# Optimization experiments

Hardware: AMD Instinct MI355X
Metric: run time of the kernel (lower is better)

The kernel has to match this reference:

```python
import jax, jax.numpy as jnp
import numpy as np

L, B, S, D, H, F = 3, 2, 2048, 256, 8, 1024
DK = D // H
EPS = 1e-7


def _positional_encoding(max_len: int, dim: int) -> jnp.ndarray:
    # pos in [1, max_len], i in [1, dim]; w = pos / 10000**((2*i//2)/dim) == pos / 10000**(i/dim)
    pos = np.arange(1, max_len + 1, dtype=np.float64)[:, None]
    i = np.arange(1, dim + 1)
    w = pos / np.power(10000.0, i.astype(np.float64) / dim)[None, :]
    pe = np.where((i % 2 == 0)[None, :], np.sin(w), np.cos(w))
    return jnp.asarray(pe, jnp.float32)


def _ln(x, g, b):
    mu = jnp.mean(x, axis=-1, keepdims=True)
    var = jnp.mean((x - mu) ** 2, axis=-1, keepdims=True)
    return (x - mu) / jnp.sqrt(var + EPS) * g + b


def setup_inputs() -> dict:
    key = jax.random.key(0)
    ks = jax.random.split(key, 16)
    s = 0.05
    inp = {
        "x": jax.random.normal(ks[0], (B, S, D), jnp.float32),
        "mask": jax.random.randint(ks[1], (B, S, S), 0, 2).astype(bool),
        "pe": _positional_encoding(S, D),
        "Wq": jax.random.normal(ks[2], (L, H, D, DK), jnp.float32) * s,
        "Wk": jax.random.normal(ks[3], (L, H, D, DK), jnp.float32) * s,
        "Wv": jax.random.normal(ks[4], (L, H, D, DK), jnp.float32) * s,
        "Wo": jax.random.normal(ks[5], (L, D, D), jnp.float32) * s,
        "bo": jnp.zeros((L, D), jnp.float32),
        "ln1_g": jnp.ones((L, D), jnp.float32),
        "ln1_b": jnp.zeros((L, D), jnp.float32),
        "W1": jax.random.normal(ks[6], (L, D, F), jnp.float32) * s,
        "b1": jnp.zeros((L, F), jnp.float32),
        "W2": jax.random.normal(ks[7], (L, F, D), jnp.float32) * s,
        "b2": jnp.zeros((L, D), jnp.float32),
        "ln2_g": jnp.ones((L, D), jnp.float32),
        "ln2_b": jnp.zeros((L, D), jnp.float32),
    }
    return inp


def _encoder_layer(x, mask, Wq, Wk, Wv, Wo, bo, ln1_g, ln1_b, W1, b1, W2, b2, ln2_g, ln2_b):
    # all heads batched: [B,S,D] x [H,D,dk] -> [B,H,S,dk]
    q = jnp.einsum('bsd,hdk->bhsk', x, Wq)
    k = jnp.einsum('bsd,hdk->bhsk', x, Wk)
    v = jnp.einsum('bsd,hdk->bhsk', x, Wv)
    scores = jnp.einsum('bhsk,bhtk->bhst', q, k) / jnp.sqrt(jnp.float32(DK))
    neg = -jnp.finfo(jnp.float32).max
    scores = jnp.where(mask[:, None, :, :], neg, scores)
    attn = jax.nn.softmax(scores, axis=-1)
    # concat heads along feature dim (head-major order as torch.cat dim=2)
    o = jnp.einsum('bhst,bhtv->bshv', attn, v).reshape(x.shape[0], x.shape[1], D)
    o = o @ Wo + bo
    x = _ln(o + x, ln1_g, ln1_b)  # post-norm (prenorm=False), dropout_rate=0
    h = jax.nn.relu(x @ W1 + b1) @ W2 + b2
    x = _ln(h + x, ln2_g, ln2_b)
    return x


def reference(x, mask, pe, Wq, Wk, Wv, Wo, bo, ln1_g, ln1_b, W1, b1, W2, b2, ln2_g, ln2_b):
    x = x + pe[None, : x.shape[1], :]
    for l in range(L):
        x = _encoder_layer(x, mask, Wq[l], Wk[l], Wv[l], Wo[l], bo[l], ln1_g[l], ln1_b[l],
                           W1[l], b1[l], W2[l], b2[l], ln2_g[l], ln2_b[l])
    return x
```

## Files before the change

### kernel.cpp

```cpp
#include <hip/hip_runtime.h>
#include <hip/hip_bf16.h>
#include <cfloat>

#define Lc 3
#define Bc 2
#define Sc 2048
#define Dc 256
#define Hc 8
#define DKc 32
#define Fc 1024

typedef __hip_bfloat16 bf16;
typedef short s8v __attribute__((ext_vector_type(8)));
typedef float f4v __attribute__((ext_vector_type(4)));

#define QSCALE 0.25504526036067815f

#if __has_builtin(__builtin_amdgcn_exp2f)
#define EXP2(x) __builtin_amdgcn_exp2f(x)
#else
#define EXP2(x) exp2f(x)
#endif

__device__ __forceinline__ float load_f(const void* p, size_t i, int isbf)
{
    return isbf ? __bfloat162float(((const bf16*)p)[i]) : ((const float*)p)[i];
}

typedef const __attribute__((address_space(1))) char gchar_t;
typedef __attribute__((address_space(3))) char lchar_t;
__device__ __forceinline__ void glds16(const void* g, void* l)
{
    __builtin_amdgcn_global_load_lds((gchar_t*)(size_t)g, (lchar_t*)(size_t)l,
                                     16, 0, 0);
}

#define NBLK_REPACK 2304
#define NBLK_CONV   6942
#define NBLK_PACK   1024
#define NBLK_PE     4096

__global__ __launch_bounds__(256) void prologue_fused(
    const void* __restrict__ x, const void* __restrict__ mask,
    const void* __restrict__ pe,
    const void* Wq, const void* Wk, const void* Wv,
    const void* Wo, const void* W1, const void* W2,
    const void* bo, const void* b1, const void* b2,
    const void* g1, const void* be1, const void* g2, const void* be2,
    bf16* __restrict__ wqkv, bf16* __restrict__ dstb, float* __restrict__ pc,
    unsigned* __restrict__ pmask, float* __restrict__ xf,
    bf16* __restrict__ xb, int* __restrict__ flags)
{
    __shared__ int sf[2];
    int tid = threadIdx.x;
    if (tid < 64) {
        const unsigned short* u16 = (const unsigned short*)x;
        int cnt = 0;
        for (int i = tid; i < 256; i += 64) {
            unsigned e = (u16[2 * i] >> 7) & 0xFF;
            cnt += (e >= 90 && e <= 140) ? 1 : 0;
        }
        #pragma unroll
        for (int d = 1; d < 64; d <<= 1) cnt += __shfl_xor(cnt, d);
        const unsigned* mu = (const unsigned*)mask;
        int c2 = ((mu[tid] & 0xFFFFFF00u) == 0) ? 1 : 0;
        #pragma unroll
        for (int d = 1; d < 64; d <<= 1) c2 += __shfl_xor(c2, d);
        if (tid == 0) {
            sf[0] = (cnt >= 128) ? 1 : 0;
            sf[1] = (c2 >= 48) ? 1 : 0;
            if (blockIdx.x == 0) { flags[0] = sf[0]; flags[1] = sf[1]; }
        }
    }
    __syncthreads();
    int isbf = sf[0], mf = sf[1];
    int blk = blockIdx.x;

    if (blk < NBLK_REPACK) {
        int idx = blk * 256 + tid;
        int l   = idx / (3 * Dc * Dc);
        int rem = idx % (3 * Dc * Dc);
        int col = rem / Dc;
        int d   = rem % Dc;
        int mat = col / Dc;
        int hk  = col % Dc;
        int h = hk / DKc, kk = hk % DKc;
        const void* W = (mat == 0) ? Wq : (mat == 1) ? Wk : Wv;
        float v = load_f(W, (size_t)l * (Hc * Dc * DKc) + h * (Dc * DKc) + d * DKc + kk, isbf);
        wqkv[idx] = __float2bfloat16(v);
    } else if (blk < NBLK_REPACK + NBLK_CONV) {
        const int NB0 = Lc * Dc * Dc;
        const int NB1 = NB0 + Lc * Dc * Fc;
        const int NB2 = NB1 + Lc * Fc * Dc;
        int idx = (blk - NBLK_REPACK) * 256 + tid;
        if (idx < NB2) {
            const void* src; int off;
            if (idx < NB0) {
                int l = idx / (Dc * Dc); int rem = idx % (Dc * Dc);
                int n = rem / Dc, k = rem % Dc;
                src = Wo; off = l * Dc * Dc + k * Dc + n;
            } else if (idx < NB1) {
                int j = idx - NB0;
                int l = j / (Fc * Dc); int rem = j % (Fc * Dc);
                int n = rem / Dc, k = rem % Dc;
                src = W1; off = l * Dc * Fc + k * Fc + n;
            } else {
                int j = idx - NB1;
                int l = j / (Dc * Fc); int rem = j % (Dc * Fc);
                int n = rem / Fc, k = rem % Fc;
                src = W2; off = l * Fc * Dc + k * Dc + n;
            }
            dstb[idx] = __float2bfloat16(load_f(src, off, isbf));
        } else {
            int off = idx - NB2;
            if (off < 7680) {
                const void* src; int lo;
                if (off < 768)       { src = bo;  lo = off; }
                else if (off < 3840) { src = b1;  lo = off - 768; }
                else if (off < 4608) { src = b2;  lo = off - 3840; }
                else if (off < 5376) { src = g1;  lo = off - 4608; }
                else if (off < 6144) { src = be1; lo = off - 5376; }
                else if (off < 6912) { src = g2;  lo = off - 6144; }
                else                 { src = be2; lo = off - 6912; }
                pc[off] = load_f(src, lo, isbf);
            }
        }
    } else if (blk < NBLK_REPACK + NBLK_CONV + NBLK_PACK) {
        int idx = (blk - NBLK_REPACK - NBLK_CONV) * 256 + tid;
        unsigned wb = 0;
        if (mf) {
            const int* mp = (const int*)mask + (size_t)idx * 32;
            #pragma unroll
            for (int u = 0; u < 8; ++u) {
                uint4 q = *(const uint4*)(mp + u * 4);
                wb |= (q.x ? 1u : 0u) << (u * 4);
                wb |= (q.y ? 1u : 0u) << (u * 4 + 1);
                wb |= (q.z ? 1u : 0u) << (u * 4 + 2);
                wb |= (q.w ? 1u : 0u) << (u * 4 + 3);
            }
        } else {
            const unsigned char* mp = (const unsigned char*)mask + (size_t)idx * 32;
            uint4 a = *(const uint4*)mp;
            uint4 bq = *(const uint4*)(mp + 16);
            const unsigned char* ab = (const unsigned char*)&a;
            const unsigned char* bb = (const unsigned char*)&bq;
            #pragma unroll
            for (int j = 0; j < 16; ++j) {
                wb |= (ab[j] ? 1u : 0u) << j;
                wb |= (bb[j] ? 1u : 0u) << (16 + j);
            }
        }
        pmask[idx] = wb;
    } else {
        int idx = (blk - NBLK_REPACK - NBLK_CONV - NBLK_PACK) * 256 + tid;
        int rem = idx % (Sc * Dc);
        float v = load_f(x, idx, isbf) + load_f(pe, rem, isbf);
        xf[idx] = v;
        xb[idx] = __float2bfloat16(v);
    }
}

__global__ __launch_bounds__(256) void gemm_mfma(
    const bf16* __restrict__ A, const bf16* __restrict__ BT,
    const float* __restrict__ bias, void* __restrict__ C,
    bf16* __restrict__ vt,
    int M, int N, int K, int relu, int obf, float ascale, int scale_ncols,
    int ldc)
{
    __shared__ __align__(16) short As[2][4096];
    __shared__ __align__(16) short Bs[2][4096];
    int tid = threadIdx.x;
    int w = tid >> 6, lane = tid & 63;
    int quad = lane >> 4, l15 = lane & 15;
    int wm0 = (w & 1) * 32, wn0 = (w >> 1) * 32;
    int row0 = blockIdx.y * 64, col0 = blockIdx.x * 64;

    int s0 = w * 128 + lane;
    int s1 = s0 + 64;
    int r0 = s0 >> 3, c0 = ((s0 & 7) ^ (r0 & 7)) * 8;
    int r1 = s1 >> 3, c1 = ((s1 & 7) ^ (r1 & 7)) * 8;
    const bf16* Ag0 = A + (size_t)(row0 + r0) * K + c0;
    const bf16* Ag1 = A + (size_t)(row0 + r1) * K + c1;
    const bf16* Bg0 = BT + (size_t)(col0 + r0) * K + c0;
    const bf16* Bg1 = BT + (size_t)(col0 + r1) * K + c1;

    f4v acc00 = {0.f,0.f,0.f,0.f}, acc01 = acc00, acc10 = acc00, acc11 = acc00;

    int m0 = wm0 + l15, m1 = wm0 + 16 + l15;
    int n0 = wn0 + l15, n1 = wn0 + 16 + l15;
    int sw7 = l15 & 7;

#define GSTAGE(bi, kk) do { \
        glds16(Ag0 + (kk), As[bi] + w * 1024); \
        glds16(Ag1 + (kk), As[bi] + w * 1024 + 512); \
        glds16(Bg0 + (kk), Bs[bi] + w * 1024); \
        glds16(Bg1 + (kk), Bs[bi] + w * 1024 + 512); \
    } while (0)

    GSTAGE(0, 0);
    for (int k0 = 0; k0 < K; k0 += 64) {
        int cur = (k0 >> 6) & 1;
        __syncthreads();
        if (k0 + 64 < K) GSTAGE(cur ^ 1, k0 + 64);
        const short* Ab = As[cur];
        const short* Bb = Bs[cur];
        #pragma unroll
        for (int kc = 0; kc < 2; ++kc) {
            int sw = ((kc * 4 + quad) ^ sw7) * 8;
            s8v a0 = *(const s8v*)(Ab + m0 * 64 + sw);
            s8v a1 = *(const s8v*)(Ab + m1 * 64 + sw);
            s8v b0 = *(const s8v*)(Bb + n0 * 64 + sw);
            s8v b1 = *(const s8v*)(Bb + n1 * 64 + sw);
            acc00 = __builtin_amdgcn_mfma_f32_16x16x32_bf16(a0, b0, acc00, 0, 0, 0);
            acc01 = __builtin_amdgcn_mfma_f32_16x16x32_bf16(a0, b1, acc01, 0, 0, 0);
            acc10 = __builtin_amdgcn_mfma_f32_16x16x32_bf16(a1, b0, acc10, 0, 0, 0);
            acc11 = __builtin_amdgcn_mfma_f32_16x16x32_bf16(a1, b1, acc11, 0, 0, 0);
        }
    }
#undef GSTAGE

    f4v accs[2][2] = {{acc00, acc01}, {acc10, acc11}};

    if (vt && col0 >= 2 * Dc) {
        __syncthreads();
        #pragma unroll
        for (int mt = 0; mt < 2; ++mt) {
            #pragma unroll
            for (int nt = 0; nt < 2; ++nt) {
                int lc = wn0 + nt * 16 + l15;
                #pragma unroll
                for (int reg = 0; reg < 4; ++reg) {
                    int lr = wm0 + mt * 16 + quad * 4 + reg;
                    int p = ((lr & 15) << 2) | (lr >> 4);
                    bf16 bv = __float2bfloat16(accs[mt][nt][reg]);
                    As[0][lc * 64 + (p ^ ((lc & 7) << 3))] = *(short*)&bv;
                }
            }
        }
        __syncthreads();
        int bI = row0 >> 11;
        int srow = row0 & (Sc - 1);
        #pragma unroll
        for (int j = 0; j < 2; ++j) {
            int e = j * 256 + tid;
            int c = e >> 3, p0 = (e & 7) * 8;
            s8v vv = *(const s8v*)(As[0] + c * 64 + (p0 ^ ((c & 7) << 3)));
            int gcv = col0 - 2 * Dc + c;
            size_t vb = ((size_t)(bI * Hc + (gcv >> 5)) * DKc + (gcv & 31)) * Sc
                        + srow + p0;
            *(s8v*)(vt + vb) = vv;
        }
        return;
    }

    float bv0 = bias ? bias[col0 + wn0 + l15] : 0.f;
    float bv1 = bias ? bias[col0 + wn0 + 16 + l15] : 0.f;
    #pragma unroll
    for (int mt = 0; mt < 2; ++mt) {
        #pragma unroll
        for (int nt = 0; nt < 2; ++nt) {
            int gr = row0 + wm0 + mt * 16 + quad * 4;
            int gc = col0 + wn0 + nt * 16 + l15;
            float badd = nt ? bv1 : bv0;
            float sc = (gc < scale_ncols) ? ascale : 1.f;
            #pragma unroll
            for (int reg = 0; reg < 4; ++reg) {
                float v = accs[mt][nt][reg] * sc + badd;
                if (relu) v = fmaxf(v, 0.f);
                if (obf) ((bf16*)C)[(size_t)(gr + reg) * ldc + gc] = __float2bfloat16(v);
                else     ((float*)C)[(size_t)(gr + reg) * ldc + gc] = v;
            }
        }
    }
}

__global__ __launch_bounds__(256) void gemm_mfma32(
    const bf16* __restrict__ A, const bf16* __restrict__ BT,
    const float* __restrict__ bias, void* __restrict__ C,
    int M, int N, int K, int relu, int obf)
{
    __shared__ __align__(16) short As[2][2048];
    __shared__ __align__(16) short Bs[2][4096];
    int tid = threadIdx.x;
    int w = tid >> 6, lane = tid & 63;
    int quad = lane >> 4, l15 = lane & 15;
    int wm0 = (w & 1) * 16, wn0 = (w >> 1) * 32;
    int row0 = blockIdx.y * 32, col0 = blockIdx.x * 64;

    int sa = w * 64 + lane;
    int ra = sa >> 3, ca = ((sa & 7) ^ (ra & 7)) * 8;
    int s0 = w * 128 + lane, s1 = s0 + 64;
    int r0 = s0 >> 3, c0 = ((s0 & 7) ^ (r0 & 7)) * 8;
    int r1 = s1 >> 3, c1 = ((s1 & 7) ^ (r1 & 7)) * 8;
    const bf16* Ag  = A + (size_t)(row0 + ra) * K + ca;
    const bf16* Bg0 = BT + (size_t)(col0 + r0) * K + c0;
    const bf16* Bg1 = BT + (size_t)(col0 + r1) * K + c1;

    f4v acc0 = {0.f,0.f,0.f,0.f}, acc1 = acc0;

    int m0 = wm0 + l15;
    int n0 = wn0 + l15, n1 = wn0 + 16 + l15;
    int sw7 = l15 & 7;

#define GSTAGE32(bi, kk) do { \
        glds16(Ag + (kk), As[bi] + w * 512); \
        glds16(Bg0 + (kk), Bs[bi] + w * 1024); \
        glds16(Bg1 + (kk), Bs[bi] + w * 1024 + 512); \
    } while (0)

    GSTAGE32(0, 0);
    for (int k0 = 0; k0 < K; k0 += 64) {
        int cur = (k0 >> 6) & 1;
        __syncthreads();
        if (k0 + 64 < K) GSTAGE32(cur ^ 1, k0 + 64);
        const short* Ab = As[cur];
        const short* Bb = Bs[cur];
        #pragma unroll
        for (int kc = 0; kc < 2; ++kc) {
            int sw = ((kc * 4 + quad) ^ sw7) * 8;
            s8v a0 = *(const s8v*)(Ab + m0 * 64 + sw);
            s8v b0 = *(const s8v*)(Bb + n0 * 64 + sw);
            s8v b1 = *(const s8v*)(Bb + n1 * 64 + sw);
            acc0 = __builtin_amdgcn_mfma_f32_16x16x32_bf16(a0, b0, acc0, 0, 0, 0);
            acc1 = __builtin_amdgcn_mfma_f32_16x16x32_bf16(a0, b1, acc1, 0, 0, 0);
        }
    }
#undef GSTAGE32

    float bv0 = bias ? bias[col0 + wn0 + l15] : 0.f;
    float bv1 = bias ? bias[col0 + wn0 + 16 + l15] : 0.f;
    f4v accs[2] = {acc0, acc1};
    #pragma unroll
    for (int nt = 0; nt < 2; ++nt) {
        int gr = row0 + wm0 + quad * 4;
        int gc = col0 + wn0 + nt * 16 + l15;
        float badd = nt ? bv1 : bv0;
        #pragma unroll
        for (int reg = 0; reg < 4; ++reg) {
            float v = accs[nt][reg] + badd;
            if (relu) v = fmaxf(v, 0.f);
            if (obf) ((bf16*)C)[(size_t)(gr + reg) * N + gc] = __float2bfloat16(v);
            else     ((float*)C)[(size_t)(gr + reg) * N + gc] = v;
        }
    }
}

__global__ __launch_bounds__(256) void flash_mfma(
    const bf16* __restrict__ qkv, const bf16* __restrict__ vt,
    const unsigned* __restrict__ pmask,
    bf16* __restrict__ op0, bf16* __restrict__ op1,
    bf16* __restrict__ op2, bf16* __restrict__ op3,
    float* __restrict__ spart)
{
    __shared__ __align__(16) short Ks[2][2048];
    __shared__ __align__(16) short Vs[2][2048];
    __shared__ __align__(16) short Pw[4][16 * 72];

    int tid = threadIdx.x;
    int w = tid >> 6;
    int lane = tid & 63;
    int quad = lane >> 4, l15 = lane & 15;
    int q0 = blockIdx.x * 64;
    int h = blockIdx.y;
    int z = blockIdx.z;
    int b = z >> 2, rng = z & 3;
    bf16* op = (rng == 0) ? op0 : (rng == 1) ? op1 : (rng == 2) ? op2 : op3;

    s8v qfrag = *(const s8v*)(qkv + (size_t)(b * Sc + q0 + w * 16 + l15) * 512 + h * 32 + quad * 8);

    int sr = tid >> 3, ss = tid & 7;
    int c8 = ss ^ (sr & 7);
    const bf16* kg = qkv + (size_t)(b * Sc + rng * (Sc / 4) + 2 * sr + (c8 >> 2)) * 512
                     + 256 + h * 32 + (c8 & 3) * 8;
    const bf16* vg = vt + ((size_t)(b * Hc + h) * DKc + sr) * Sc + rng * (Sc / 4) + c8 * 8;

    int koff = (l15 >> 1) * 64 + ((((l15 & 1) << 2) + quad) ^ ((l15 >> 1) & 7)) * 8;
    int pfoff = l15 * 72 + quad * 8;
    int vkey = l15 & 7;
    int voff = l15 * 64;

    f4v o0 = {0.f,0.f,0.f,0.f}, o1 = o0;
    float ssum[4] = {0.f, 0.f, 0.f, 0.f};

    short* pwv = Pw[w];
    const unsigned* mp = pmask + (size_t)b * Sc * (Sc / 32)
                         + (size_t)(q0 + w * 16 + quad * 4) * (Sc / 32) + rng * 16;

#define FSTAGE(bi, it2) do { \
        glds16(kg + (size_t)(it2) * (64 * 512), Ks[bi] + w * 512); \
        glds16(vg + (it2) * 64, Vs[bi] + w * 512); \
    } while (0)

    FSTAGE(0, 0);
    for (int it = 0; it < 8; ++it) {
        int cur = it & 1;
        __syncthreads();
        if (it < 7) FSTAGE(cur ^ 1, it + 1);

        uint2 mw[4];
        #pragma unroll
        for (int reg = 0; reg < 4; ++reg)
            mw[reg] = *(const uint2*)(mp + reg * (Sc / 32) + it * 2);

        const short* kb = Ks[cur];
        f4v sfr[4];
        __builtin_amdgcn_s_setprio(1);
        #pragma unroll
        for (int nt = 0; nt < 4; ++nt) {
            s8v kf = *(const s8v*)(kb + koff + nt * 512);
            f4v zz = {0.f,0.f,0.f,0.f};
            sfr[nt] = __builtin_amdgcn_mfma_f32_16x16x32_bf16(qfrag, kf, zz, 0, 0, 0);
        }
        __builtin_amdgcn_s_setprio(0);
        #pragma unroll
        for (int reg = 0; reg < 4; ++reg) {
            unsigned ta = mw[reg].x >> l15;
            unsigned tb = mw[reg].y >> l15;
            float p0 = EXP2(sfr[0][reg]); if (ta & 1u)         p0 = 0.f;
            float p1 = EXP2(sfr[1][reg]); if ((ta >> 16) & 1u) p1 = 0.f;
            float p2 = EXP2(sfr[2][reg]); if (tb & 1u)         p2 = 0.f;
            float p3 = EXP2(sfr[3][reg]); if ((tb >> 16) & 1u) p3 = 0.f;
            ssum[reg] += (p0 + p1) + (p2 + p3);
            __hip_bfloat162 plo = __float22bfloat162_rn(make_float2(p0, p1));
            __hip_bfloat162 phi = __float22bfloat162_rn(make_float2(p2, p3));
            uint2 pk = {*(unsigned*)&plo, *(unsigned*)&phi};
            *(uint2*)(pwv + (quad * 4 + reg) * 72 + l15 * 4) = pk;
        }
        const short* vb = Vs[cur];
        __builtin_amdgcn_s_setprio(1);
        #pragma unroll
        for (int kc = 0; kc < 2; ++kc) {
            s8v pf = *(const s8v*)(pwv + pfoff + kc * 32);
            int vo = voff + (((kc * 4 + quad) ^ vkey) * 8);
            s8v vf0 = *(const s8v*)(vb + vo);
            s8v vf1 = *(const s8v*)(vb + vo + 1024);
            o0 = __builtin_amdgcn_mfma_f32_16x16x32_bf16(pf, vf0, o0, 0, 0, 0);
            o1 = __builtin_amdgcn_mfma_f32_16x16x32_bf16(pf, vf1, o1, 0, 0, 0);
        }
        __builtin_amdgcn_s_setprio(0);
    }
#undef FSTAGE

    #pragma unroll
    for (int reg = 0; reg < 4; ++reg) {
        #pragma unroll
        for (int d = 1; d < 16; d <<= 1) ssum[reg] += __shfl_xor(ssum[reg], d);
    }

    #pragma unroll
    for (int reg = 0; reg < 4; ++reg) {
        int row = q0 + w * 16 + quad * 4 + reg;
        size_t ob = (size_t)(b * Sc + row) * Dc + h * DKc;
        op[ob + l15]      = __float2bfloat16(o0[reg]);
        op[ob + 16 + l15] = __float2bfloat16(o1[reg]);
        if (l15 == 0)
            spart[((size_t)(rng * Bc + b) * Hc + h) * Sc + row] = ssum[reg];
    }
}

__global__ __launch_bounds__(256) void attn_merge(
    const bf16* __restrict__ op0, const bf16* __restrict__ op1,
    const bf16* __restrict__ op2, const bf16* __restrict__ op3,
    const float* __restrict__ spart, bf16* __restrict__ attn_out)
{
    int t8 = blockIdx.x * 256 + threadIdx.x;
    size_t idx = (size_t)t8 * 8;
    int d = (int)(idx & 255);
    int h = d >> 5;
    int row = (int)((idx >> 8) & (Sc - 1));
    int b = (int)(idx >> 19);
    float s = 0.f;
    #pragma unroll
    for (int r = 0; r < 4; ++r)
        s += spart[((size_t)(r * Bc + b) * Hc + h) * Sc + row];
    float inv = 1.f / fmaxf(s, 1e-30f);

    uint4 a0 = *(const uint4*)(op0 + idx);
    uint4 a1 = *(const uint4*)(op1 + idx);
    uint4 a2 = *(const uint4*)(op2 + idx);
    uint4 a3 = *(const uint4*)(op3 + idx);
    const unsigned short* u0 = (const unsigned short*)&a0;
    const unsigned short* u1 = (const unsigned short*)&a1;
    const unsigned short* u2 = (const unsigned short*)&a2;
    const unsigned short* u3 = (const unsigned short*)&a3;
    unsigned short outv[8];
    #pragma unroll
    for (int j = 0; j < 8; ++j) {
        float o = (__uint_as_float((unsigned)u0[j] << 16) + __uint_as_float((unsigned)u1[j] << 16))
                + (__uint_as_float((unsigned)u2[j] << 16) + __uint_as_float((unsigned)u3[j] << 16));
        bf16 ov = __float2bfloat16(o * inv);
        outv[j] = *(unsigned short*)&ov;
    }
    *(uint4*)(attn_out + idx) = *(uint4*)outv;
}

__global__ __launch_bounds__(256) void add_ln(
    const float* __restrict__ a, float* __restrict__ xf, bf16* __restrict__ xb,
    const float* __restrict__ g, const float* __restrict__ b,
    void* __restrict__ dout, const int* __restrict__ flags)
{
    __shared__ float ws4[2][4];
    int row = blockIdx.x, d = threadIdx.x;
    size_t idx = (size_t)row * Dc + d;
    float v = a[idx] + xf[idx];
    float s = v;
    #pragma unroll
    for (int dd = 1; dd < 64; dd <<= 1) s += __shfl_xor(s, dd);
    if ((d & 63) == 0) ws4[0][d >> 6] = s;
    __syncthreads();
    float mu = (ws4[0][0] + ws4[0][1] + ws4[0][2] + ws4[0][3]) * (1.f / Dc);
    float c = v - mu;
    float q = c * c;
    #pragma unroll
    for (int dd = 1; dd < 64; dd <<= 1) q += __shfl_xor(q, dd);
    if ((d & 63) == 0) ws4[1][d >> 6] = q;
    __syncthreads();
    float var = (ws4[1][0] + ws4[1][1] + ws4[1][2] + ws4[1][3]) * (1.f / Dc);
    float r2 = c * rsqrtf(var + 1e-7f) * g[d] + b[d];
    xf[idx] = r2;
    xb[idx] = __float2bfloat16(r2);
    if (dout) {
        if (flags[0]) ((bf16*)dout)[idx] = __float2bfloat16(r2);
        else          ((float*)dout)[idx] = r2;
    }
}

extern "C" void kernel_launch(void* const* d_in, const int* in_sizes, int n_in,
                              void* d_out, int out_size, void* d_ws, size_t ws_size,
                              hipStream_t stream)
{
    const void* x    = d_in[0];
    const void* mask = d_in[1];
    const void* pe   = d_in[2];
    const void* Wq   = d_in[3];
    const void* Wk   = d_in[4];
    const void* Wv   = d_in[5];
    const void* Wo   = d_in[6];
    const void* bo   = d_in[7];
    const void* ln1g = d_in[8];
    const void* ln1b = d_in[9];
    const void* W1   = d_in[10];
    const void* b1   = d_in[11];
    const void* W2   = d_in[12];
    const void* b2   = d_in[13];
    const void* ln2g = d_in[14];
    const void* ln2b = d_in[15];

    const int M = Bc * Sc;
    char* ws = (char*)d_ws;
    const size_t MB = 1024 * 1024;
    int*      flags    = (int*)ws;
    float*    xf32     = (float*)(ws + 256);
    float*    obuf     = (float*)(ws + 256 + 4 * MB);
    char*     bigc     = ws + 256 + 8 * MB;
    bf16*     xbf      = (bf16*)(ws + 256 + 16 * MB);
    bf16*     attn_out = (bf16*)(ws + 256 + 18 * MB);
    bf16*     wqkv     = (bf16*)(ws + 256 + 20 * MB);
    bf16*     woc      = wqkv + (size_t)Lc * Dc * 3 * Dc;
    bf16*     w1c      = woc + (size_t)Lc * Dc * Dc;
    bf16*     w2c      = w1c + (size_t)Lc * Dc * Fc;
    float*    pc       = (float*)(w2c + (size_t)Lc * Fc * Dc);
    unsigned* pmask    = (unsigned*)(ws + 256 + 25 * MB);
    float*    spart    = (float*)(ws + 256 + 26 * MB);

    bf16* qkv  = (bf16*)bigc;
    bf16* vtb  = (bf16*)(bigc + 4 * MB);
    bf16* hbuf = (bf16*)bigc;
    bf16* op0  = (bf16*)obuf;
    bf16* op1  = op0 + (size_t)M * Dc;
    bf16* op2  = attn_out;
    bf16* op3  = (bf16*)(bigc + 6 * MB);

    float* pc_bo   = pc;
    float* pc_b1   = pc + 768;
    float* pc_b2   = pc + 3840;
    float* pc_ln1g = pc + 4608;
    float* pc_ln1b = pc + 5376;
    float* pc_ln2g = pc + 6144;
    float* pc_ln2b = pc + 6912;

    prologue_fused<<<NBLK_REPACK + NBLK_CONV + NBLK_PACK + NBLK_PE, 256, 0, stream>>>(
        x, mask, pe, Wq, Wk, Wv, Wo, W1, W2, bo, b1, b2,
        ln1g, ln1b, ln2g, ln2b, wqkv, woc, pc, pmask, xf32, xbf, flags);

    for (int l = 0; l < Lc; ++l) {
        gemm_mfma<<<dim3(3 * Dc / 64, M / 64), 256, 0, stream>>>(
            xbf, wqkv + (size_t)l * Dc * 3 * Dc, nullptr, qkv, vtb,
            M, 3 * Dc, Dc, 0, 1, QSCALE, Dc, 512);
        flash_mfma<<<dim3(Sc / 64, Hc, Bc * 4), 256, 0, stream>>>(
            qkv, vtb, pmask, op0, op1, op2, op3, spart);
        attn_merge<<<(Bc * Sc * Dc / 8) / 256, 256, 0, stream>>>(
            op0, op1, op2, op3, spart, attn_out);
        gemm_mfma32<<<dim3(Dc / 64, M / 32), 256, 0, stream>>>(
            attn_out, woc + (size_t)l * Dc * Dc, pc_bo + l * Dc, obuf, M, Dc, Dc, 0, 0);
        add_ln<<<M, 256, 0, stream>>>(obuf, xf32, xbf,
            pc_ln1g + l * Dc, pc_ln1b + l * Dc, nullptr, flags);
        gemm_mfma<<<dim3(Fc / 64, M / 64), 256, 0, stream>>>(
            xbf, w1c + (size_t)l * Dc * Fc, pc_b1 + l * Fc, hbuf, nullptr,
            M, Fc, Dc, 1, 1, 1.f, 0, Fc);
        gemm_mfma32<<<dim3(Dc / 64, M / 32), 256, 0, stream>>>(
            hbuf, w2c + (size_t)l * Fc * Dc, pc_b2 + l * Dc, obuf, M, Dc, Fc, 0, 0);
        add_ln<<<M, 256, 0, stream>>>(obuf, xf32, xbf,
            pc_ln2g + l * Dc, pc_ln2b + l * Dc,
            (l == Lc - 1) ? d_out : nullptr, flags);
    }
}
```

Baseline: 343.5 us.

## Triple-buffer K/V tiles in flash attention with explicit vmcnt waits and mask prefetch

Moves the flash attention K/V staging from a double buffer to a triple buffer, issuing loads two tiles ahead. It replaces __syncthreads with explicit s_waitcnt vmcnt counts plus a raw s_barrier, fully unrolls the loop, and prefetches the next tile's mask words into registers. The goal is to hide global-to-LDS latency and mask load latency behind MFMA work. In exchange it uses more LDS, which can lower occupancy. The hand-counted vmcnt values must match the real number of outstanding loads or the kernel will read stale data.

```diff
diff --git a/kernel.cpp b/kernel.cpp
--- a/kernel.cpp
+++ b/kernel.cpp
@@ -352,8 +352,8 @@
     bf16* __restrict__ op2, bf16* __restrict__ op3,
     float* __restrict__ spart)
 {
-    __shared__ __align__(16) short Ks[2][2048];
-    __shared__ __align__(16) short Vs[2][2048];
+    __shared__ __align__(16) short Ks[3][2048];
+    __shared__ __align__(16) short Vs[3][2048];
     __shared__ __align__(16) short Pw[4][16 * 72];
 
     int tid = threadIdx.x;
@@ -391,18 +391,29 @@
         glds16(vg + (it2) * 64, Vs[bi] + w * 512); \
     } while (0)
 
+    uint2 mwc[4], mwn[4];
+    #pragma unroll
+    for (int reg = 0; reg < 4; ++reg)
+        mwc[reg] = *(const uint2*)(mp + reg * (Sc / 32));
     FSTAGE(0, 0);
+    FSTAGE(1, 1);
+
+    #pragma unroll
     for (int it = 0; it < 8; ++it) {
-        int cur = it & 1;
-        __syncthreads();
-        if (it < 7) FSTAGE(cur ^ 1, it + 1);
-
-        uint2 mw[4];
-        #pragma unroll
-        for (int reg = 0; reg < 4; ++reg)
-            mw[reg] = *(const uint2*)(mp + reg * (Sc / 32) + it * 2);
-
-        const short* kb = Ks[cur];
+        if (it < 7) {
+            #pragma unroll
+            for (int reg = 0; reg < 4; ++reg)
+                mwn[reg] = *(const uint2*)(mp + reg * (Sc / 32) + (it + 1) * 2);
+            asm volatile("s_waitcnt vmcnt(6)" ::: "memory");
+        } else {
+            asm volatile("s_waitcnt vmcnt(0)" ::: "memory");
+        }
+        __builtin_amdgcn_sched_barrier(0);
+        __builtin_amdgcn_s_barrier();
+        __builtin_amdgcn_sched_barrier(0);
+        if (it + 2 < 8) FSTAGE((it + 2) % 3, it + 2);
+
+        const short* kb = Ks[it % 3];
         f4v sfr[4];
         __builtin_amdgcn_s_setprio(1);
         #pragma unroll
@@ -414,8 +425,8 @@
         __builtin_amdgcn_s_setprio(0);
         #pragma unroll
         for (int reg = 0; reg < 4; ++reg) {
-            unsigned ta = mw[reg].x >> l15;
-            unsigned tb = mw[reg].y >> l15;
+            unsigned ta = mwc[reg].x >> l15;
+            unsigned tb = mwc[reg].y >> l15;
             float p0 = EXP2(sfr[0][reg]); if (ta & 1u)         p0 = 0.f;
             float p1 = EXP2(sfr[1][reg]); if ((ta >> 16) & 1u) p1 = 0.f;
             float p2 = EXP2(sfr[2][reg]); if (tb & 1u)         p2 = 0.f;
@@ -426,7 +437,7 @@
             uint2 pk = {*(unsigned*)&plo, *(unsigned*)&phi};
             *(uint2*)(pwv + (quad * 4 + reg) * 72 + l15 * 4) = pk;
         }
-        const short* vb = Vs[cur];
+        const short* vb = Vs[it % 3];
         __builtin_amdgcn_s_setprio(1);
         #pragma unroll
         for (int kc = 0; kc < 2; ++kc) {
@@ -438,6 +449,8 @@
             o1 = __builtin_amdgcn_mfma_f32_16x16x32_bf16(pf, vf1, o1, 0, 0, 0);
         }
         __builtin_amdgcn_s_setprio(0);
+        #pragma unroll
+        for (int reg = 0; reg < 4; ++reg) mwc[reg] = mwn[reg];
     }
 #undef FSTAGE
 
```

New measurement: 348.8 us. No clear change (+1.5%).

## Drop split-K attention and merge kernel; process all keys per block

Applied to the files above, without the earlier changes.

The flash attention kernel no longer splits the key range into four parts. Each block now iterates over all 2048 keys and normalizes its output directly, and the separate merge kernel with its partial buffers is removed. This saves the partial-output writes and reads plus one launch per layer. In exchange the attention grid has a quarter as many blocks, which lowers occupancy and parallelism on the GPU.

```diff
diff --git a/kernel.cpp b/kernel.cpp
--- a/kernel.cpp
+++ b/kernel.cpp
@@ -347,10 +347,7 @@
 
 __global__ __launch_bounds__(256) void flash_mfma(
     const bf16* __restrict__ qkv, const bf16* __restrict__ vt,
-    const unsigned* __restrict__ pmask,
-    bf16* __restrict__ op0, bf16* __restrict__ op1,
-    bf16* __restrict__ op2, bf16* __restrict__ op3,
-    float* __restrict__ spart)
+    const unsigned* __restrict__ pmask, bf16* __restrict__ attn_out)
 {
     __shared__ __align__(16) short Ks[2][2048];
     __shared__ __align__(16) short Vs[2][2048];
@@ -362,17 +359,15 @@
     int quad = lane >> 4, l15 = lane & 15;
     int q0 = blockIdx.x * 64;
     int h = blockIdx.y;
-    int z = blockIdx.z;
-    int b = z >> 2, rng = z & 3;
-    bf16* op = (rng == 0) ? op0 : (rng == 1) ? op1 : (rng == 2) ? op2 : op3;
+    int b = blockIdx.z;
 
     s8v qfrag = *(const s8v*)(qkv + (size_t)(b * Sc + q0 + w * 16 + l15) * 512 + h * 32 + quad * 8);
 
     int sr = tid >> 3, ss = tid & 7;
     int c8 = ss ^ (sr & 7);
-    const bf16* kg = qkv + (size_t)(b * Sc + rng * (Sc / 4) + 2 * sr + (c8 >> 2)) * 512
+    const bf16* kg = qkv + (size_t)(b * Sc + 2 * sr + (c8 >> 2)) * 512
                      + 256 + h * 32 + (c8 & 3) * 8;
-    const bf16* vg = vt + ((size_t)(b * Hc + h) * DKc + sr) * Sc + rng * (Sc / 4) + c8 * 8;
+    const bf16* vg = vt + ((size_t)(b * Hc + h) * DKc + sr) * Sc + c8 * 8;
 
     int koff = (l15 >> 1) * 64 + ((((l15 & 1) << 2) + quad) ^ ((l15 >> 1) & 7)) * 8;
     int pfoff = l15 * 72 + quad * 8;
@@ -384,7 +379,7 @@
 
     short* pwv = Pw[w];
     const unsigned* mp = pmask + (size_t)b * Sc * (Sc / 32)
-                         + (size_t)(q0 + w * 16 + quad * 4) * (Sc / 32) + rng * 16;
+                         + (size_t)(q0 + w * 16 + quad * 4) * (Sc / 32);
 
 #define FSTAGE(bi, it2) do { \
         glds16(kg + (size_t)(it2) * (64 * 512), Ks[bi] + w * 512); \
@@ -392,10 +387,10 @@
     } while (0)
 
     FSTAGE(0, 0);
-    for (int it = 0; it < 8; ++it) {
+    for (int it = 0; it < 32; ++it) {
         int cur = it & 1;
         __syncthreads();
-        if (it < 7) FSTAGE(cur ^ 1, it + 1);
+        if (it < 31) FSTAGE(cur ^ 1, it + 1);
 
         uint2 mw[4];
         #pragma unroll
@@ -451,47 +446,10 @@
     for (int reg = 0; reg < 4; ++reg) {
         int row = q0 + w * 16 + quad * 4 + reg;
         size_t ob = (size_t)(b * Sc + row) * Dc + h * DKc;
-        op[ob + l15]      = __float2bfloat16(o0[reg]);
-        op[ob + 16 + l15] = __float2bfloat16(o1[reg]);
-        if (l15 == 0)
-            spart[((size_t)(rng * Bc + b) * Hc + h) * Sc + row] = ssum[reg];
-    }
-}
-
-__global__ __launch_bounds__(256) void attn_merge(
-    const bf16* __restrict__ op0, const bf16* __restrict__ op1,
-    const bf16* __restrict__ op2, const bf16* __restrict__ op3,
-    const float* __restrict__ spart, bf16* __restrict__ attn_out)
-{
-    int t8 = blockIdx.x * 256 + threadIdx.x;
-    size_t idx = (size_t)t8 * 8;
-    int d = (int)(idx & 255);
-    int h = d >> 5;
-    int row = (int)((idx >> 8) & (Sc - 1));
-    int b = (int)(idx >> 19);
-    float s = 0.f;
-    #pragma unroll
-    for (int r = 0; r < 4; ++r)
-        s += spart[((size_t)(r * Bc + b) * Hc + h) * Sc + row];
-    float inv = 1.f / fmaxf(s, 1e-30f);
-
-    uint4 a0 = *(const uint4*)(op0 + idx);
-    uint4 a1 = *(const uint4*)(op1 + idx);
-    uint4 a2 = *(const uint4*)(op2 + idx);
-    uint4 a3 = *(const uint4*)(op3 + idx);
-    const unsigned short* u0 = (const unsigned short*)&a0;
-    const unsigned short* u1 = (const unsigned short*)&a1;
-    const unsigned short* u2 = (const unsigned short*)&a2;
-    const unsigned short* u3 = (const unsigned short*)&a3;
-    unsigned short outv[8];
-    #pragma unroll
-    for (int j = 0; j < 8; ++j) {
-        float o = (__uint_as_float((unsigned)u0[j] << 16) + __uint_as_float((unsigned)u1[j] << 16))
-                + (__uint_as_float((unsigned)u2[j] << 16) + __uint_as_float((unsigned)u3[j] << 16));
-        bf16 ov = __float2bfloat16(o * inv);
-        outv[j] = *(unsigned short*)&ov;
-    }
-    *(uint4*)(attn_out + idx) = *(uint4*)outv;
+        float inv = 1.f / fmaxf(ssum[reg], 1e-30f);
+        attn_out[ob + l15]      = __float2bfloat16(o0[reg] * inv);
+        attn_out[ob + 16 + l15] = __float2bfloat16(o1[reg] * inv);
+    }
 }
 
 __global__ __launch_bounds__(256) void add_ln(
@@ -561,15 +519,10 @@
     bf16*     w2c      = w1c + (size_t)Lc * Dc * Fc;
     float*    pc       = (float*)(w2c + (size_t)Lc * Fc * Dc);
     unsigned* pmask    = (unsigned*)(ws + 256 + 25 * MB);
-    float*    spart    = (float*)(ws + 256 + 26 * MB);
 
     bf16* qkv  = (bf16*)bigc;
     bf16* vtb  = (bf16*)(bigc + 4 * MB);
     bf16* hbuf = (bf16*)bigc;
-    bf16* op0  = (bf16*)obuf;
-    bf16* op1  = op0 + (size_t)M * Dc;
-    bf16* op2  = attn_out;
-    bf16* op3  = (bf16*)(bigc + 6 * MB);
 
     float* pc_bo   = pc;
     float* pc_b1   = pc + 768;
@@ -587,10 +540,8 @@
         gemm_mfma<<<dim3(3 * Dc / 64, M / 64), 256, 0, stream>>>(
             xbf, wqkv + (size_t)l * Dc * 3 * Dc, nullptr, qkv, vtb,
             M, 3 * Dc, Dc, 0, 1, QSCALE, Dc, 512);
-        flash_mfma<<<dim3(Sc / 64, Hc, Bc * 4), 256, 0, stream>>>(
-            qkv, vtb, pmask, op0, op1, op2, op3, spart);
-        attn_merge<<<(Bc * Sc * Dc / 8) / 256, 256, 0, stream>>>(
-            op0, op1, op2, op3, spart, attn_out);
+        flash_mfma<<<dim3(Sc / 64, Hc, Bc), 256, 0, stream>>>(
+            qkv, vtb, pmask, attn_out);
         gemm_mfma32<<<dim3(Dc / 64, M / 32), 256, 0, stream>>>(
             attn_out, woc + (size_t)l * Dc * Dc, pc_bo + l * Dc, obuf, M, Dc, Dc, 0, 0);
         add_ln<<<M, 256, 0, stream>>>(obuf, xf32, xbf,
```

Measured after the change: 351.2 us. +2.2%, slower.

## Fuse attention merge into Wo GEMM, split-K FFN2, MFMA row sums

Applied to the files above, without the earlier changes.

Removes the separate attn_merge kernel by having a new gemm_wo kernel read the four partial attention outputs, sum them, normalise by the combined softmax row sums, and write the merged bf16 tile straight into shared memory as its A operand. The W2 GEMM is split along K into two z-slices writing separate fp32 buffers, which add_ln then sums, raising block count for this small-N GEMM. Flash attention now computes its row sums with an extra MFMA against a vector of ones instead of scalar adds and shuffles. The changes save one launch and one intermediate round trip through memory, at the cost of redundant merge work across column blocks in gemm_wo and an extra fp32 buffer read in add_ln.

```diff
diff --git a/kernel.cpp b/kernel.cpp
--- a/kernel.cpp
+++ b/kernel.cpp
@@ -276,8 +276,9 @@
 
 __global__ __launch_bounds__(256) void gemm_mfma32(
     const bf16* __restrict__ A, const bf16* __restrict__ BT,
-    const float* __restrict__ bias, void* __restrict__ C,
-    int M, int N, int K, int relu, int obf)
+    const float* __restrict__ bias, float* __restrict__ C0,
+    float* __restrict__ C1,
+    int M, int N, int Kfull, int Ksub)
 {
     __shared__ __align__(16) short As[2][2048];
     __shared__ __align__(16) short Bs[2][4096];
@@ -286,15 +287,16 @@
     int quad = lane >> 4, l15 = lane & 15;
     int wm0 = (w & 1) * 16, wn0 = (w >> 1) * 32;
     int row0 = blockIdx.y * 32, col0 = blockIdx.x * 64;
-
-    int sa = w * 64 + lane;
-    int ra = sa >> 3, ca = ((sa & 7) ^ (ra & 7)) * 8;
+    int kbase = blockIdx.z * Ksub;
+    float* C = blockIdx.z ? C1 : C0;
+
+    int ra = tid >> 3, ca = ((tid & 7) ^ (ra & 7)) * 8;
     int s0 = w * 128 + lane, s1 = s0 + 64;
     int r0 = s0 >> 3, c0 = ((s0 & 7) ^ (r0 & 7)) * 8;
     int r1 = s1 >> 3, c1 = ((s1 & 7) ^ (r1 & 7)) * 8;
-    const bf16* Ag  = A + (size_t)(row0 + ra) * K + ca;
-    const bf16* Bg0 = BT + (size_t)(col0 + r0) * K + c0;
-    const bf16* Bg1 = BT + (size_t)(col0 + r1) * K + c1;
+    const bf16* Ag  = A + (size_t)(row0 + ra) * Kfull + kbase + ca;
+    const bf16* Bg0 = BT + (size_t)(col0 + r0) * Kfull + kbase + c0;
+    const bf16* Bg1 = BT + (size_t)(col0 + r1) * Kfull + kbase + c1;
 
     f4v acc0 = {0.f,0.f,0.f,0.f}, acc1 = acc0;
 
@@ -309,10 +311,10 @@
     } while (0)
 
     GSTAGE32(0, 0);
-    for (int k0 = 0; k0 < K; k0 += 64) {
+    for (int k0 = 0; k0 < Ksub; k0 += 64) {
         int cur = (k0 >> 6) & 1;
         __syncthreads();
-        if (k0 + 64 < K) GSTAGE32(cur ^ 1, k0 + 64);
+        if (k0 + 64 < Ksub) GSTAGE32(cur ^ 1, k0 + 64);
         const short* Ab = As[cur];
         const short* Bb = Bs[cur];
         #pragma unroll
@@ -327,8 +329,9 @@
     }
 #undef GSTAGE32
 
-    float bv0 = bias ? bias[col0 + wn0 + l15] : 0.f;
-    float bv1 = bias ? bias[col0 + wn0 + 16 + l15] : 0.f;
+    int addb = (blockIdx.z == 0) && bias;
+    float bv0 = addb ? bias[col0 + wn0 + l15] : 0.f;
+    float bv1 = addb ? bias[col0 + wn0 + 16 + l15] : 0.f;
     f4v accs[2] = {acc0, acc1};
     #pragma unroll
     for (int nt = 0; nt < 2; ++nt) {
@@ -336,12 +339,114 @@
         int gc = col0 + wn0 + nt * 16 + l15;
         float badd = nt ? bv1 : bv0;
         #pragma unroll
-        for (int reg = 0; reg < 4; ++reg) {
-            float v = accs[nt][reg] + badd;
-            if (relu) v = fmaxf(v, 0.f);
-            if (obf) ((bf16*)C)[(size_t)(gr + reg) * N + gc] = __float2bfloat16(v);
-            else     ((float*)C)[(size_t)(gr + reg) * N + gc] = v;
-        }
+        for (int reg = 0; reg < 4; ++reg)
+            C[(size_t)(gr + reg) * N + gc] = accs[nt][reg] + badd;
+    }
+}
+
+__global__ __launch_bounds__(256) void gemm_wo(
+    const bf16* __restrict__ op0, const bf16* __restrict__ op1,
+    const bf16* __restrict__ op2, const bf16* __restrict__ op3,
+    const float* __restrict__ spart,
+    const bf16* __restrict__ BT, const float* __restrict__ bias,
+    float* __restrict__ C)
+{
+    __shared__ __align__(16) short As[2][2048];
+    __shared__ __align__(16) short Bs[2][4096];
+    int tid = threadIdx.x;
+    int w = tid >> 6, lane = tid & 63;
+    int quad = lane >> 4, l15 = lane & 15;
+    int wm0 = (w & 1) * 16, wn0 = (w >> 1) * 32;
+    int row0 = blockIdx.y * 32, col0 = blockIdx.x * 64;
+
+    int ra = tid >> 3, ca = ((tid & 7) ^ (ra & 7)) * 8;
+    int gr = row0 + ra;
+    int bI = gr >> 11, srow = gr & (Sc - 1);
+    const bf16* a0p = op0 + (size_t)gr * Dc + ca;
+    const bf16* a1p = op1 + (size_t)gr * Dc + ca;
+    const bf16* a2p = op2 + (size_t)gr * Dc + ca;
+    const bf16* a3p = op3 + (size_t)gr * Dc + ca;
+    const float* sp = spart + (size_t)bI * Hc * Sc + srow;
+
+    int s0 = w * 128 + lane, s1 = s0 + 64;
+    int r0 = s0 >> 3, c0 = ((s0 & 7) ^ (r0 & 7)) * 8;
+    int r1 = s1 >> 3, c1 = ((s1 & 7) ^ (r1 & 7)) * 8;
+    const bf16* Bg0 = BT + (size_t)(col0 + r0) * Dc + c0;
+    const bf16* Bg1 = BT + (size_t)(col0 + r1) * Dc + c1;
+
+    f4v acc0 = {0.f,0.f,0.f,0.f}, acc1 = acc0;
+    int m0 = wm0 + l15;
+    int n0 = wn0 + l15, n1 = wn0 + 16 + l15;
+    int sw7 = l15 & 7;
+
+    uint4 u0, u1, u2, u3;
+    float inv;
+
+#define AREGS(kk) do { \
+        int hh = ((kk) + ca) >> 5; \
+        float s = (sp[(size_t)hh * Sc] + sp[(size_t)(Bc * Hc + hh) * Sc]) \
+                + (sp[(size_t)(2 * Bc * Hc + hh) * Sc] + sp[(size_t)(3 * Bc * Hc + hh) * Sc]); \
+        inv = 1.f / fmaxf(s, 1e-30f); \
+        u0 = *(const uint4*)(a0p + (kk)); u1 = *(const uint4*)(a1p + (kk)); \
+        u2 = *(const uint4*)(a2p + (kk)); u3 = *(const uint4*)(a3p + (kk)); \
+    } while (0)
+
+#define AWRITE(bi) do { \
+        const unsigned short* q0 = (const unsigned short*)&u0; \
+        const unsigned short* q1 = (const unsigned short*)&u1; \
+        const unsigned short* q2 = (const unsigned short*)&u2; \
+        const unsigned short* q3 = (const unsigned short*)&u3; \
+        unsigned short ov[8]; \
+        _Pragma("unroll") \
+        for (int j = 0; j < 8; ++j) { \
+            float f = (__uint_as_float((unsigned)q0[j] << 16) + __uint_as_float((unsigned)q1[j] << 16)) \
+                    + (__uint_as_float((unsigned)q2[j] << 16) + __uint_as_float((unsigned)q3[j] << 16)); \
+            bf16 bv = __float2bfloat16(f * inv); \
+            ov[j] = *(unsigned short*)&bv; \
+        } \
+        *(uint4*)(As[bi] + (size_t)tid * 8) = *(uint4*)ov; \
+    } while (0)
+
+    AREGS(0);
+    glds16(Bg0, Bs[0] + w * 1024);
+    glds16(Bg1, Bs[0] + w * 1024 + 512);
+    AWRITE(0);
+
+    for (int k0 = 0; k0 < Dc; k0 += 64) {
+        int cur = (k0 >> 6) & 1;
+        __syncthreads();
+        if (k0 + 64 < Dc) {
+            glds16(Bg0 + k0 + 64, Bs[cur ^ 1] + w * 1024);
+            glds16(Bg1 + k0 + 64, Bs[cur ^ 1] + w * 1024 + 512);
+            AREGS(k0 + 64);
+        }
+        const short* Ab = As[cur];
+        const short* Bb = Bs[cur];
+        #pragma unroll
+        for (int kc = 0; kc < 2; ++kc) {
+            int sw = ((kc * 4 + quad) ^ sw7) * 8;
+            s8v a0 = *(const s8v*)(Ab + m0 * 64 + sw);
+            s8v b0 = *(const s8v*)(Bb + n0 * 64 + sw);
+            s8v b1 = *(const s8v*)(Bb + n1 * 64 + sw);
+            acc0 = __builtin_amdgcn_mfma_f32_16x16x32_bf16(a0, b0, acc0, 0, 0, 0);
+            acc1 = __builtin_amdgcn_mfma_f32_16x16x32_bf16(a0, b1, acc1, 0, 0, 0);
+        }
+        if (k0 + 64 < Dc) AWRITE(cur ^ 1);
+    }
+#undef AREGS
+#undef AWRITE
+
+    float bv0 = bias ? bias[col0 + wn0 + l15] : 0.f;
+    float bv1 = bias ? bias[col0 + wn0 + 16 + l15] : 0.f;
+    f4v accs[2] = {acc0, acc1};
+    #pragma unroll
+    for (int nt = 0; nt < 2; ++nt) {
+        int grr = row0 + wm0 + quad * 4;
+        int gc = col0 + wn0 + nt * 16 + l15;
+        float badd = nt ? bv1 : bv0;
+        #pragma unroll
+        for (int reg = 0; reg < 4; ++reg)
+            C[(size_t)(grr + reg) * Dc + gc] = accs[nt][reg] + badd;
     }
 }
 
@@ -379,8 +484,10 @@
     int vkey = l15 & 7;
     int voff = l15 * 64;
 
-    f4v o0 = {0.f,0.f,0.f,0.f}, o1 = o0;
-    float ssum[4] = {0.f, 0.f, 0.f, 0.f};
+    f4v o0 = {0.f,0.f,0.f,0.f}, o1 = o0, ssa = o0;
+    s8v ones;
+    #pragma unroll
+    for (int j = 0; j < 8; ++j) ones[j] = (short)0x3F80;
 
     short* pwv = Pw[w];
     const unsigned* mp = pmask + (size_t)b * Sc * (Sc / 32)
@@ -420,7 +527,6 @@
             float p1 = EXP2(sfr[1][reg]); if ((ta >> 16) & 1u) p1 = 0.f;
             float p2 = EXP2(sfr[2][reg]); if (tb & 1u)         p2 = 0.f;
             float p3 = EXP2(sfr[3][reg]); if ((tb >> 16) & 1u) p3 = 0.f;
-            ssum[reg] += (p0 + p1) + (p2 + p3);
             __hip_bfloat162 plo = __float22bfloat162_rn(make_float2(p0, p1));
             __hip_bfloat162 phi = __float22bfloat162_rn(make_float2(p2, p3));
             uint2 pk = {*(unsigned*)&plo, *(unsigned*)&phi};
@@ -434,18 +540,13 @@
             int vo = voff + (((kc * 4 + quad) ^ vkey) * 8);
             s8v vf0 = *(const s8v*)(vb + vo);
             s8v vf1 = *(const s8v*)(vb + vo + 1024);
-            o0 = __builtin_amdgcn_mfma_f32_16x16x32_bf16(pf, vf0, o0, 0, 0, 0);
-            o1 = __builtin_amdgcn_mfma_f32_16x16x32_bf16(pf, vf1, o1, 0, 0, 0);
+            o0  = __builtin_amdgcn_mfma_f32_16x16x32_bf16(pf, vf0, o0, 0, 0, 0);
+            o1  = __builtin_amdgcn_mfma_f32_16x16x32_bf16(pf, vf1, o1, 0, 0, 0);
+            ssa = __builtin_amdgcn_mfma_f32_16x16x32_bf16(pf, ones, ssa, 0, 0, 0);
         }
         __builtin_amdgcn_s_setprio(0);
     }
 #undef FSTAGE
-
-    #pragma unroll
-    for (int reg = 0; reg < 4; ++reg) {
-        #pragma unroll
-        for (int d = 1; d < 16; d <<= 1) ssum[reg] += __shfl_xor(ssum[reg], d);
-    }
 
     #pragma unroll
     for (int reg = 0; reg < 4; ++reg) {
@@ -454,48 +555,13 @@
         op[ob + l15]      = __float2bfloat16(o0[reg]);
         op[ob + 16 + l15] = __float2bfloat16(o1[reg]);
         if (l15 == 0)
-            spart[((size_t)(rng * Bc + b) * Hc + h) * Sc + row] = ssum[reg];
-    }
-}
-
-__global__ __launch_bounds__(256) void attn_merge(
-    const bf16* __restrict__ op0, const bf16* __restrict__ op1,
-    const bf16* __restrict__ op2, const bf16* __restrict__ op3,
-    const float* __restrict__ spart, bf16* __restrict__ attn_out)
-{
-    int t8 = blockIdx.x * 256 + threadIdx.x;
-    size_t idx = (size_t)t8 * 8;
-    int d = (int)(idx & 255);
-    int h = d >> 5;
-    int row = (int)((idx >> 8) & (Sc - 1));
-    int b = (int)(idx >> 19);
-    float s = 0.f;
-    #pragma unroll
-    for (int r = 0; r < 4; ++r)
-        s += spart[((size_t)(r * Bc + b) * Hc + h) * Sc + row];
-    float inv = 1.f / fmaxf(s, 1e-30f);
-
-    uint4 a0 = *(const uint4*)(op0 + idx);
-    uint4 a1 = *(const uint4*)(op1 + idx);
-    uint4 a2 = *(const uint4*)(op2 + idx);
-    uint4 a3 = *(const uint4*)(op3 + idx);
-    const unsigned short* u0 = (const unsigned short*)&a0;
-    const unsigned short* u1 = (const unsigned short*)&a1;
-    const unsigned short* u2 = (const unsigned short*)&a2;
-    const unsigned short* u3 = (const unsigned short*)&a3;
-    unsigned short outv[8];
-    #pragma unroll
-    for (int j = 0; j < 8; ++j) {
-        float o = (__uint_as_float((unsigned)u0[j] << 16) + __uint_as_float((unsigned)u1[j] << 16))
-                + (__uint_as_float((unsigned)u2[j] << 16) + __uint_as_float((unsigned)u3[j] << 16));
-        bf16 ov = __float2bfloat16(o * inv);
-        outv[j] = *(unsigned short*)&ov;
-    }
-    *(uint4*)(attn_out + idx) = *(uint4*)outv;
+            spart[((size_t)(rng * Bc + b) * Hc + h) * Sc + row] = ssa[reg];
+    }
 }
 
 __global__ __launch_bounds__(256) void add_ln(
-    const float* __restrict__ a, float* __restrict__ xf, bf16* __restrict__ xb,
+    const float* __restrict__ a, const float* __restrict__ a2,
+    float* __restrict__ xf, bf16* __restrict__ xb,
     const float* __restrict__ g, const float* __restrict__ b,
     void* __restrict__ dout, const int* __restrict__ flags)
 {
@@ -503,6 +569,7 @@
     int row = blockIdx.x, d = threadIdx.x;
     size_t idx = (size_t)row * Dc + d;
     float v = a[idx] + xf[idx];
+    if (a2) v += a2[idx];
     float s = v;
     #pragma unroll
     for (int dd = 1; dd < 64; dd <<= 1) s += __shfl_xor(s, dd);
@@ -554,7 +621,6 @@
     float*    obuf     = (float*)(ws + 256 + 4 * MB);
     char*     bigc     = ws + 256 + 8 * MB;
     bf16*     xbf      = (bf16*)(ws + 256 + 16 * MB);
-    bf16*     attn_out = (bf16*)(ws + 256 + 18 * MB);
     bf16*     wqkv     = (bf16*)(ws + 256 + 20 * MB);
     bf16*     woc      = wqkv + (size_t)Lc * Dc * 3 * Dc;
     bf16*     w1c      = woc + (size_t)Lc * Dc * Dc;
@@ -562,14 +628,15 @@
     float*    pc       = (float*)(w2c + (size_t)Lc * Fc * Dc);
     unsigned* pmask    = (unsigned*)(ws + 256 + 25 * MB);
     float*    spart    = (float*)(ws + 256 + 26 * MB);
+    bf16*     op0      = (bf16*)(ws + 28 * MB);
+    bf16*     op1      = (bf16*)(ws + 30 * MB);
+    bf16*     op2      = (bf16*)(ws + 32 * MB);
+    bf16*     op3      = (bf16*)(ws + 34 * MB);
+    float*    obuf1    = (float*)(ws + 36 * MB);
 
     bf16* qkv  = (bf16*)bigc;
     bf16* vtb  = (bf16*)(bigc + 4 * MB);
     bf16* hbuf = (bf16*)bigc;
-    bf16* op0  = (bf16*)obuf;
-    bf16* op1  = op0 + (size_t)M * Dc;
-    bf16* op2  = attn_out;
-    bf16* op3  = (bf16*)(bigc + 6 * MB);
 
     float* pc_bo   = pc;
     float* pc_b1   = pc + 768;
@@ -589,18 +656,18 @@
             M, 3 * Dc, Dc, 0, 1, QSCALE, Dc, 512);
         flash_mfma<<<dim3(Sc / 64, Hc, Bc * 4), 256, 0, stream>>>(
             qkv, vtb, pmask, op0, op1, op2, op3, spart);
-        attn_merge<<<(Bc * Sc * Dc / 8) / 256, 256, 0, stream>>>(
-            op0, op1, op2, op3, spart, attn_out);
-        gemm_mfma32<<<dim3(Dc / 64, M / 32), 256, 0, stream>>>(
-            attn_out, woc + (size_t)l * Dc * Dc, pc_bo + l * Dc, obuf, M, Dc, Dc, 0, 0);
-        add_ln<<<M, 256, 0, stream>>>(obuf, xf32, xbf,
+        gemm_wo<<<dim3(Dc / 64, M / 32), 256, 0, stream>>>(
+            op0, op1, op2, op3, spart, woc + (size_t)l * Dc * Dc,
+            pc_bo + l * Dc, obuf);
+        add_ln<<<M, 256, 0, stream>>>(obuf, nullptr, xf32, xbf,
             pc_ln1g + l * Dc, pc_ln1b + l * Dc, nullptr, flags);
         gemm_mfma<<<dim3(Fc / 64, M / 64), 256, 0, stream>>>(
             xbf, w1c + (size_t)l * Dc * Fc, pc_b1 + l * Fc, hbuf, nullptr,
             M, Fc, Dc, 1, 1, 1.f, 0, Fc);
-        gemm_mfma32<<<dim3(Dc / 64, M / 32), 256, 0, stream>>>(
-            hbuf, w2c + (size_t)l * Fc * Dc, pc_b2 + l * Dc, obuf, M, Dc, Fc, 0, 0);
-        add_ln<<<M, 256, 0, stream>>>(obuf, xf32, xbf,
+        gemm_mfma32<<<dim3(Dc / 64, M / 32, 2), 256, 0, stream>>>(
+            hbuf, w2c + (size_t)l * Fc * Dc, pc_b2 + l * Dc, obuf, obuf1,
+            M, Dc, Fc, Fc / 2);
+        add_ln<<<M, 256, 0, stream>>>(obuf, obuf1, xf32, xbf,
             pc_ln2g + l * Dc, pc_ln2b + l * Dc,
             (l == Lc - 1) ? d_out : nullptr, flags);
     }
```

Measured after the change: 334.9 us. 1.03x faster.
